# Kernel tuning notes

Hardware: AMD Instinct MI355X
Metric: run time of the kernel (lower is better)

The kernel has to match this reference:

```python
import jax, jax.numpy as jnp
import numpy as np

EPS = 1e-12  # F.normalize eps


def setup_inputs() -> dict:
    key = jax.random.key(0)
    k1, k2, k3 = jax.random.split(key, 3)
    N, C, H, W, K = 64, 512, 28, 28, 64
    x = jax.random.normal(k1, (N, C, H, W), dtype=jnp.float32)
    conv_w = jax.random.normal(k2, (K, C), dtype=jnp.float32)  # 1x1 conv weight squeezed
    centroids = jax.random.uniform(k3, (K, C), dtype=jnp.float32)  # torch.rand init
    return {"x": x, "conv_w": conv_w, "centroids": centroids}


def reference(x, conv_w, centroids):
    N, C, H, W = x.shape
    K = centroids.shape[0]
    xf = x.reshape(N, C, H * W)                                  # (N, C, L)
    # 1x1 conv == matmul over channels, softmax over cluster dim
    logits = jnp.einsum('kc,ncl->nkl', conv_w, xf)               # (N, K, L)
    a = jax.nn.softmax(logits, axis=1)                           # softmax over clusters
    # vlad[n,k,c] = sum_l a[n,k,l] * (x[n,c,l] - cent[k,c])
    #            = (a @ x^T)[n,k,c] - (sum_l a[n,k,l]) * cent[k,c]
    agg = jnp.einsum('nkl,ncl->nkc', a, xf)                      # (N, K, C)
    vlad = agg - a.sum(axis=-1)[..., None] * centroids[None]     # (N, K, C)
    # intra-normalize per cluster (dim=2)
    vlad = vlad / jnp.maximum(jnp.linalg.norm(vlad, axis=2, keepdims=True), EPS)
    v = vlad.reshape(N, K * C)
    # global L2 normalize
    v = v / jnp.maximum(jnp.linalg.norm(v, axis=1, keepdims=True), EPS)
    return v
```

## Files before the change

### kernel.cpp

```cpp
#include <hip/hip_runtime.h>

#define C_ 512
#define L_ 784
#define K_ 64
#define EPS_ 1e-12f

typedef _Float16 half_t;
typedef _Float16 half8 __attribute__((ext_vector_type(8)));
typedef _Float16 half4 __attribute__((ext_vector_type(4)));
typedef float float4v __attribute__((ext_vector_type(4)));

__global__ __launch_bounds__(1024) void kF(const float* __restrict__ x,
                                           const float* __restrict__ w,
                                           float* __restrict__ aggP,
                                           float* __restrict__ asumP) {
    __shared__ half_t wh[64 * 520];
    __shared__ half_t xt[16 * 520];
    __shared__ float  sl[4352];
    __shared__ half_t ah[64 * 40];
    __shared__ float  asb[16 * 64];

    const int t    = threadIdx.x;
    const int n    = blockIdx.y;
    const int bx   = blockIdx.x;
    const int l0   = bx * 192;
    const int NT   = (bx == 3) ? 13 : 12;
    const int wv   = t >> 6;
    const int lane = t & 63;
    const int n16  = lane & 15;
    const int q    = lane >> 4;

    const float* xn = x + (size_t)n * (C_ * L_);

#pragma unroll
    for (int i = 0; i < 8; ++i) {
        int e  = t + 1024 * i;
        int k  = e >> 7;
        int cq = e & 127;
        float4v f = *(const float4v*)(w + (size_t)k * C_ + 4 * cq);
        *(half4*)&wh[k * 520 + 4 * cq] =
            half4{(half_t)f.x, (half_t)f.y, (half_t)f.z, (half_t)f.w};
    }

    {
        const int l  = t & 15;
        const int cg = t >> 4;
        const float* src = xn + l0 + l;
        float v0[8];
#pragma unroll
        for (int j = 0; j < 8; ++j) v0[j] = src[(size_t)(8 * cg + j) * L_];
        half8 h;
#pragma unroll
        for (int j = 0; j < 8; ++j) h[j] = (half_t)v0[j];
        *(half8*)&xt[l * 520 + 8 * cg] = h;
    }

    float4v agc[8];
#pragma unroll
    for (int i = 0; i < 8; ++i) agc[i] = float4v{0.f, 0.f, 0.f, 0.f};
    float asum_reg = 0.f;

    const int kt  = wv & 3;
    const int cs  = wv >> 2;
    const int kt2 = wv & 3;
    const int cg2 = wv >> 2;

    __syncthreads();

    float pre[8];
    for (int s = 0; s < NT; ++s) {
        if (s + 1 < NT) {
            const float* src = xn + l0 + (s + 1) * 16 + (t & 15);
            const int cg = t >> 4;
#pragma unroll
            for (int j = 0; j < 8; ++j) pre[j] = src[(size_t)(8 * cg + j) * L_];
        }
        {
            float4v lac = {0.f, 0.f, 0.f, 0.f};
#pragma unroll
            for (int st = 0; st < 4; ++st) {
                const int c0 = cs * 128 + st * 32;
                half8 A = *(const half8*)&xt[n16 * 520 + c0 + 8 * q];
                half8 B = *(const half8*)&wh[(kt * 16 + n16) * 520 + c0 + 8 * q];
                lac = __builtin_amdgcn_mfma_f32_16x16x32_f16(A, B, lac, 0, 0, 0);
            }
#pragma unroll
            for (int r = 0; r < 4; ++r)
                sl[cs * 1088 + (4 * q + r) * 68 + kt * 16 + n16] = lac[r];
        }
        __syncthreads();
        {
            float lg = sl[wv * 68 + lane] + sl[1088 + wv * 68 + lane] +
                       sl[2176 + wv * 68 + lane] + sl[3264 + wv * 68 + lane];
            float mx = lg;
#pragma unroll
            for (int off = 32; off; off >>= 1) mx = fmaxf(mx, __shfl_xor(mx, off, 64));
            float e  = __expf(lg - mx);
            float sm = e;
#pragma unroll
            for (int off = 32; off; off >>= 1) sm += __shfl_xor(sm, off, 64);
            float a = e / sm;
            asum_reg += a;
            ah[lane * 40 + (s & 1) * 16 + wv] = (half_t)a;
        }
        if (s + 1 < NT) {
            half8 h;
#pragma unroll
            for (int j = 0; j < 8; ++j) h[j] = (half_t)pre[j];
            *(half8*)&xt[(t & 15) * 520 + 8 * (t >> 4)] = h;
        }
        __syncthreads();
        const bool tail_single = (s == NT - 1) && ((s & 1) == 0);
        if (tail_single) {
            ah[(t >> 4) * 40 + 16 + (t & 15)] = (half_t)0.f;
            __syncthreads();
        }
        if ((s & 1) || tail_single) {
            const int l0p = l0 + (s & ~1) * 16;
#pragma unroll
            for (int i = 0; i < 8; ++i) {
                const int c = (cg2 * 8 + i) * 16 + n16;
                int bl = l0p + 8 * q;
                if (bl > 776) bl = 776;
                const float* xp = xn + (size_t)c * L_ + bl;
                float4v f0 = *(const float4v*)xp;
                float4v f1 = *(const float4v*)(xp + 4);
                half8 A = {(half_t)f0.x, (half_t)f0.y, (half_t)f0.z, (half_t)f0.w,
                           (half_t)f1.x, (half_t)f1.y, (half_t)f1.z, (half_t)f1.w};
                half8 B = *(const half8*)&ah[(kt2 * 16 + n16) * 40 + 8 * q];
                agc[i] = __builtin_amdgcn_mfma_f32_16x16x32_f16(A, B, agc[i], 0, 0, 0);
            }
        }
    }

    asb[wv * 64 + lane] = asum_reg;

#pragma unroll
    for (int i = 0; i < 8; ++i) {
        __syncthreads();
#pragma unroll
        for (int r = 0; r < 4; ++r)
            sl[(kt2 * 16 + n16) * 68 + cg2 * 16 + 4 * q + r] = agc[i][r];
        __syncthreads();
        const int k  = t >> 4;
        const int g  = (t >> 2) & 3;
        const int e2 = t & 3;
        float4v f = *(const float4v*)&sl[k * 68 + g * 16 + 4 * e2];
        *(float4v*)(aggP + (((size_t)n * 4 + bx) * 64 + k) * C_ +
                    g * 128 + i * 16 + 4 * e2) = f;
    }
    __syncthreads();
    if (t < 64) {
        float s_ = 0.f;
        for (int j = 0; j < 16; ++j) s_ += asb[j * 64 + t];
        asumP[((size_t)n * 4 + bx) * 64 + t] = s_;
    }
}

__global__ __launch_bounds__(256) void kC(const float* __restrict__ aggP,
                                          const float* __restrict__ cent,
                                          const float* __restrict__ asumP,
                                          float* __restrict__ out) {
    __shared__ float asumS[8];
    const int t  = threadIdx.x;
    const int n  = blockIdx.y;
    const int k0 = blockIdx.x * 8;
    if (t < 8) {
        float s = 0.f;
        for (int j = 0; j < 4; ++j) s += asumP[((size_t)n * 4 + j) * 64 + k0 + t];
        asumS[t] = s;
    }
    __syncthreads();
    const int wv   = t >> 6;
    const int lane = t & 63;
    for (int r = wv; r < 8; r += 4) {
        const int k = k0 + r;
        const float as = asumS[r];
        const float* a0 = aggP + (((size_t)n * 4 + 0) * 64 + k) * C_;
        const float* a1 = aggP + (((size_t)n * 4 + 1) * 64 + k) * C_;
        const float* a2 = aggP + (((size_t)n * 4 + 2) * 64 + k) * C_;
        const float* a3 = aggP + (((size_t)n * 4 + 3) * 64 + k) * C_;
        const float* cp = cent + (size_t)k * C_;
        float v[8];
        float ss = 0.f;
#pragma unroll
        for (int j = 0; j < 8; ++j) {
            const int c = lane + 64 * j;
            float val = a0[c] + a1[c] + a2[c] + a3[c] - as * cp[c];
            v[j] = val;
            ss += val * val;
        }
#pragma unroll
        for (int off = 32; off; off >>= 1) ss += __shfl_xor(ss, off, 64);
        const float scale = 1.f / (fmaxf(sqrtf(ss), EPS_) * 8.f);
        float* op = out + (size_t)n * (K_ * C_) + (size_t)k * C_;
#pragma unroll
        for (int j = 0; j < 8; ++j) op[lane + 64 * j] = v[j] * scale;
    }
}

extern "C" void kernel_launch(void* const* d_in, const int* in_sizes, int n_in,
                              void* d_out, int out_size, void* d_ws, size_t ws_size,
                              hipStream_t stream) {
    (void)in_sizes; (void)n_in; (void)out_size; (void)ws_size;
    const float* x    = (const float*)d_in[0];
    const float* w    = (const float*)d_in[1];
    const float* cent = (const float*)d_in[2];
    float* out = (float*)d_out;

    char* base = (char*)d_ws;
    float* aggP  = (float*)base;
    float* asumP = aggP + (size_t)64 * 4 * 64 * 512;

    kF<<<dim3(4, 64), 1024, 0, stream>>>(x, w, aggP, asumP);
    kC<<<dim3(8, 64), 256, 0, stream>>>(aggP, cent, asumP, out);
}
```

Before: 200.0 us.

## Load x tile once into LDS for both GEMMs and keep weights in registers

Each x tile is now loaded from global once, with coalesced 32-byte row reads. It is written to LDS in two layouts: a transposed copy for the logits MFMA and a double-buffered channel-major copy for the aggregation MFMA. Before, the aggregation step reloaded x from global memory a second time. The conv weights move from a large LDS array into per-lane registers, the sl stride is padded to 65, and the agg epilogue writes MFMA results straight to global without the LDS staging loop. The risks are LDS bank conflicts on the scalar transposed stores, more register pressure, and uncoalesced scalar global stores for aggP.

```diff
diff --git a/kernel.cpp b/kernel.cpp
--- a/kernel.cpp
+++ b/kernel.cpp
@@ -7,18 +7,16 @@
 
 typedef _Float16 half_t;
 typedef _Float16 half8 __attribute__((ext_vector_type(8)));
-typedef _Float16 half4 __attribute__((ext_vector_type(4)));
 typedef float float4v __attribute__((ext_vector_type(4)));
 
 __global__ __launch_bounds__(1024) void kF(const float* __restrict__ x,
                                            const float* __restrict__ w,
                                            float* __restrict__ aggP,
                                            float* __restrict__ asumP) {
-    __shared__ half_t wh[64 * 520];
     __shared__ half_t xt[16 * 520];
-    __shared__ float  sl[4352];
+    __shared__ half_t xc[2][512 * 40];
+    __shared__ float  sl[4 * 16 * 65];
     __shared__ half_t ah[64 * 40];
-    __shared__ float  asb[16 * 64];
 
     const int t    = threadIdx.x;
     const int n    = blockIdx.y;
@@ -27,32 +25,37 @@
     const int NT   = (bx == 3) ? 13 : 12;
     const int wv   = t >> 6;
     const int lane = t & 63;
-    const int n16  = lane & 15;
+    const int m16  = lane & 15;
     const int q    = lane >> 4;
+    const int kt   = wv & 3;
+    const int cs   = wv >> 2;
 
     const float* xn = x + (size_t)n * (C_ * L_);
 
-#pragma unroll
-    for (int i = 0; i < 8; ++i) {
-        int e  = t + 1024 * i;
-        int k  = e >> 7;
-        int cq = e & 127;
-        float4v f = *(const float4v*)(w + (size_t)k * C_ + 4 * cq);
-        *(half4*)&wh[k * 520 + 4 * cq] =
-            half4{(half_t)f.x, (half_t)f.y, (half_t)f.z, (half_t)f.w};
-    }
-
+    half8 wf[4];
     {
-        const int l  = t & 15;
-        const int cg = t >> 4;
-        const float* src = xn + l0 + l;
-        float v0[8];
-#pragma unroll
-        for (int j = 0; j < 8; ++j) v0[j] = src[(size_t)(8 * cg + j) * L_];
-        half8 h;
-#pragma unroll
-        for (int j = 0; j < 8; ++j) h[j] = (half_t)v0[j];
-        *(half8*)&xt[l * 520 + 8 * cg] = h;
+        const float* wr = w + (size_t)(kt * 16 + m16) * C_ + cs * 128 + 8 * q;
+#pragma unroll
+        for (int st = 0; st < 4; ++st) {
+            float4v f0 = *(const float4v*)(wr + 32 * st);
+            float4v f1 = *(const float4v*)(wr + 32 * st + 4);
+            wf[st] = half8{(half_t)f0.x, (half_t)f0.y, (half_t)f0.z, (half_t)f0.w,
+                           (half_t)f1.x, (half_t)f1.y, (half_t)f1.z, (half_t)f1.w};
+        }
+    }
+
+    const int sc  = t >> 1;
+    const int slq = t & 1;
+    const float* xs = xn + (size_t)sc * L_ + l0 + 8 * slq;
+
+    {
+        float4v f0 = *(const float4v*)xs;
+        float4v f1 = *(const float4v*)(xs + 4);
+        half8 h = {(half_t)f0.x, (half_t)f0.y, (half_t)f0.z, (half_t)f0.w,
+                   (half_t)f1.x, (half_t)f1.y, (half_t)f1.z, (half_t)f1.w};
+        *(half8*)&xc[0][sc * 40 + 8 * slq] = h;
+#pragma unroll
+        for (int j = 0; j < 8; ++j) xt[(8 * slq + j) * 520 + sc] = h[j];
     }
 
     float4v agc[8];
@@ -60,42 +63,35 @@
     for (int i = 0; i < 8; ++i) agc[i] = float4v{0.f, 0.f, 0.f, 0.f};
     float asum_reg = 0.f;
 
-    const int kt  = wv & 3;
-    const int cs  = wv >> 2;
-    const int kt2 = wv & 3;
-    const int cg2 = wv >> 2;
-
     __syncthreads();
 
-    float pre[8];
     for (int s = 0; s < NT; ++s) {
-        if (s + 1 < NT) {
-            const float* src = xn + l0 + (s + 1) * 16 + (t & 15);
-            const int cg = t >> 4;
-#pragma unroll
-            for (int j = 0; j < 8; ++j) pre[j] = src[(size_t)(8 * cg + j) * L_];
+        float4v p0, p1;
+        const bool pf = (s + 1 < NT);
+        if (pf) {
+            const float* p = xs + (s + 1) * 16;
+            p0 = *(const float4v*)p;
+            p1 = *(const float4v*)(p + 4);
         }
         {
             float4v lac = {0.f, 0.f, 0.f, 0.f};
 #pragma unroll
             for (int st = 0; st < 4; ++st) {
-                const int c0 = cs * 128 + st * 32;
-                half8 A = *(const half8*)&xt[n16 * 520 + c0 + 8 * q];
-                half8 B = *(const half8*)&wh[(kt * 16 + n16) * 520 + c0 + 8 * q];
-                lac = __builtin_amdgcn_mfma_f32_16x16x32_f16(A, B, lac, 0, 0, 0);
+                half8 A = *(const half8*)&xt[m16 * 520 + cs * 128 + st * 32 + 8 * q];
+                lac = __builtin_amdgcn_mfma_f32_16x16x32_f16(A, wf[st], lac, 0, 0, 0);
             }
 #pragma unroll
             for (int r = 0; r < 4; ++r)
-                sl[cs * 1088 + (4 * q + r) * 68 + kt * 16 + n16] = lac[r];
+                sl[cs * 1040 + (4 * q + r) * 65 + kt * 16 + m16] = lac[r];
         }
         __syncthreads();
         {
-            float lg = sl[wv * 68 + lane] + sl[1088 + wv * 68 + lane] +
-                       sl[2176 + wv * 68 + lane] + sl[3264 + wv * 68 + lane];
+            float lg = sl[wv * 65 + lane] + sl[1040 + wv * 65 + lane] +
+                       sl[2080 + wv * 65 + lane] + sl[3120 + wv * 65 + lane];
             float mx = lg;
 #pragma unroll
             for (int off = 32; off; off >>= 1) mx = fmaxf(mx, __shfl_xor(mx, off, 64));
-            float e  = __expf(lg - mx);
+            float e = __expf(lg - mx);
             float sm = e;
 #pragma unroll
             for (int off = 32; off; off >>= 1) sm += __shfl_xor(sm, off, 64);
@@ -103,58 +99,45 @@
             asum_reg += a;
             ah[lane * 40 + (s & 1) * 16 + wv] = (half_t)a;
         }
-        if (s + 1 < NT) {
-            half8 h;
-#pragma unroll
-            for (int j = 0; j < 8; ++j) h[j] = (half_t)pre[j];
-            *(half8*)&xt[(t & 15) * 520 + 8 * (t >> 4)] = h;
+        if (pf) {
+            half8 h = {(half_t)p0.x, (half_t)p0.y, (half_t)p0.z, (half_t)p0.w,
+                       (half_t)p1.x, (half_t)p1.y, (half_t)p1.z, (half_t)p1.w};
+            const int sp = s + 1;
+            *(half8*)&xc[(sp >> 1) & 1][sc * 40 + (sp & 1) * 16 + 8 * slq] = h;
+#pragma unroll
+            for (int j = 0; j < 8; ++j) xt[(8 * slq + j) * 520 + sc] = h[j];
         }
         __syncthreads();
-        const bool tail_single = (s == NT - 1) && ((s & 1) == 0);
+        const bool tail_single = (s == NT - 1) && !(s & 1);
         if (tail_single) {
             ah[(t >> 4) * 40 + 16 + (t & 15)] = (half_t)0.f;
             __syncthreads();
         }
         if ((s & 1) || tail_single) {
-            const int l0p = l0 + (s & ~1) * 16;
+            const half_t* xcb = xc[(s >> 1) & 1];
+            half8 A = *(const half8*)&ah[(kt * 16 + m16) * 40 + 8 * q];
 #pragma unroll
             for (int i = 0; i < 8; ++i) {
-                const int c = (cg2 * 8 + i) * 16 + n16;
-                int bl = l0p + 8 * q;
-                if (bl > 776) bl = 776;
-                const float* xp = xn + (size_t)c * L_ + bl;
-                float4v f0 = *(const float4v*)xp;
-                float4v f1 = *(const float4v*)(xp + 4);
-                half8 A = {(half_t)f0.x, (half_t)f0.y, (half_t)f0.z, (half_t)f0.w,
-                           (half_t)f1.x, (half_t)f1.y, (half_t)f1.z, (half_t)f1.w};
-                half8 B = *(const half8*)&ah[(kt2 * 16 + n16) * 40 + 8 * q];
+                half8 B = *(const half8*)&xcb[((cs * 8 + i) * 16 + m16) * 40 + 8 * q];
                 agc[i] = __builtin_amdgcn_mfma_f32_16x16x32_f16(A, B, agc[i], 0, 0, 0);
             }
         }
     }
 
-    asb[wv * 64 + lane] = asum_reg;
-
-#pragma unroll
-    for (int i = 0; i < 8; ++i) {
-        __syncthreads();
-#pragma unroll
-        for (int r = 0; r < 4; ++r)
-            sl[(kt2 * 16 + n16) * 68 + cg2 * 16 + 4 * q + r] = agc[i][r];
-        __syncthreads();
-        const int k  = t >> 4;
-        const int g  = (t >> 2) & 3;
-        const int e2 = t & 3;
-        float4v f = *(const float4v*)&sl[k * 68 + g * 16 + 4 * e2];
-        *(float4v*)(aggP + (((size_t)n * 4 + bx) * 64 + k) * C_ +
-                    g * 128 + i * 16 + 4 * e2) = f;
-    }
+    sl[wv * 64 + lane] = asum_reg;
     __syncthreads();
     if (t < 64) {
         float s_ = 0.f;
-        for (int j = 0; j < 16; ++j) s_ += asb[j * 64 + t];
+#pragma unroll
+        for (int j = 0; j < 16; ++j) s_ += sl[j * 64 + t];
         asumP[((size_t)n * 4 + bx) * 64 + t] = s_;
     }
+    float* ap = aggP + (((size_t)n * 4 + bx) * 64) * (size_t)C_;
+#pragma unroll
+    for (int i = 0; i < 8; ++i)
+#pragma unroll
+        for (int r = 0; r < 4; ++r)
+            ap[(size_t)(kt * 16 + 4 * q + r) * C_ + (cs * 8 + i) * 16 + m16] = agc[i][r];
 }
 
 __global__ __launch_bounds__(256) void kC(const float* __restrict__ aggP,
```

After: 183.3 us. -8.4%, faster.
